# Performance work log

Measured on AMD Instinct MI355X. Metric: run time of the kernel, lower is better.

## Reference

```python
import jax, jax.numpy as jnp
import numpy as np

LAYER_SIZES = [256, 256, 256]
SPLIT_HALF = True
B, F0, D = 512, 32, 32


def setup_inputs() -> dict:
    key = jax.random.key(0)
    ks = jax.random.split(key, 7)
    field_nums = [F0]
    for i, s in enumerate(LAYER_SIZES):
        field_nums.append(s // 2 if (SPLIT_HALF and i != len(LAYER_SIZES) - 1) else (s // 2 if SPLIT_HALF else s))
    # field_nums = [32, 128, 128, 128] (last entry unused for weights)
    inp = {
        'feat': jax.random.normal(ks[0], (B, F0, D), dtype=jnp.float32),
        'W0': jax.random.normal(ks[1], (LAYER_SIZES[0], field_nums[0], F0), dtype=jnp.float32) * 0.05,
        'b0': jnp.zeros((LAYER_SIZES[0],), dtype=jnp.float32),
        'W1': jax.random.normal(ks[2], (LAYER_SIZES[1], field_nums[1], F0), dtype=jnp.float32) * 0.05,
        'b1': jnp.zeros((LAYER_SIZES[1],), dtype=jnp.float32),
        'W2': jax.random.normal(ks[3], (LAYER_SIZES[2], field_nums[2], F0), dtype=jnp.float32) * 0.05,
        'b2': jnp.zeros((LAYER_SIZES[2],), dtype=jnp.float32),
    }
    return inp


def _cin_layer(h, feat, W, b):
    # h: [B,H,D], feat: [B,F0,D], W: [K,H,F0], b: [K] -> out [B,K,D]
    # outer product per embedding dim, then 1x1 conv (full [H,F0] contraction)
    z = jnp.einsum('bid,bjd->bdij', h, feat)          # [B,D,H,F0]
    out = jnp.einsum('bdij,kij->bkd', z, W) + b[None, :, None]
    return jax.nn.relu(out)


def reference(feat, W0, b0, W1, b1, W2, b2):
    Ws = [W0, W1, W2]
    bs = [b0, b1, b2]
    h = feat
    p = []
    n_layers = len(LAYER_SIZES)
    for l, K in enumerate(LAYER_SIZES):
        out = _cin_layer(h, feat, Ws[l], bs[l])        # [B,K,D]
        if SPLIT_HALF and l != n_layers - 1:
            h = out[:, :K // 2, :]
            direct = out[:, K // 2:, :]
        else:
            direct = out
            h = out
        p.append(direct)
    return jnp.concatenate(p, axis=1).sum(-1)          # [B, sum of direct sizes]
```

## Files before the change

kernel.cpp:

```cpp
#include <hip/hip_runtime.h>
#include <hip/hip_fp16.h>
#include <stdint.h>


typedef _Float16 half8_t __attribute__((ext_vector_type(8)));
typedef float f32x4 __attribute__((ext_vector_type(4)));
typedef uint32_t u32x4 __attribute__((ext_vector_type(4)));

union H8 {
  half8_t h;
  uint32_t u[4];
  u32x4 q;
};

#define AS1 __attribute__((address_space(1)))
#define AS3 __attribute__((address_space(3)))

static __device__ __forceinline__ uint32_t pkmul(uint32_t x, uint32_t y) {
  __half2 a = __builtin_bit_cast(__half2, x);
  __half2 b = __builtin_bit_cast(__half2, y);
  __half2 r = __hmul2(a, b);
  return __builtin_bit_cast(uint32_t, r);
}

__global__ void prep_kernel(const float* __restrict__ W0, const float* __restrict__ W1,
                            const float* __restrict__ W2, const float* __restrict__ feat,
                            uint16_t* __restrict__ Wt0, uint16_t* __restrict__ Wt1,
                            uint16_t* __restrict__ Wt2,
                            uint16_t* __restrict__ F16, uint16_t* __restrict__ Fpk) {
  int blk = blockIdx.x;
  if (blk < 4608) {
    const float* W; uint16_t* Wt; int FLsh, base;
    if (blk < 512)       { W = W0; Wt = Wt0; FLsh = 5; base = 0; }
    else if (blk < 2560) { W = W1; Wt = Wt1; FLsh = 7; base = 512; }
    else                 { W = W2; Wt = Wt2; FLsh = 7; base = 2560; }
    int idx2 = (blk - base) * 256 + threadIdx.x;
    float2 xy = *(const float2*)(W + (size_t)idx2 * 2);
    int j2 = idx2 & 15;
    int i = (idx2 >> 4) & ((1 << FLsh) - 1);
    int k = idx2 >> (4 + FLsh);
    __half2 h2 = __floats2half2_rn(xy.x, xy.y);
    int g = j2 >> 2, kr = k & 15, kt = k >> 4;
    uint32_t* wt32 = (uint32_t*)Wt;
    wt32[(((size_t)i * 16 + kt) * 64 + g * 16 + kr) * 4 + (j2 & 3)] = *(uint32_t*)&h2;
  } else {
    int m = (blk - 4608) * 256 + threadIdx.x;
    int b = m >> 5, d = m & 31;
    const float* fb = feat + (size_t)b * 1024 + d;
    uint16_t hs[32];
#pragma unroll
    for (int j = 0; j < 32; ++j)
      hs[j] = __half_as_ushort(__float2half(fb[j * 32]));
    int mt = m >> 6, g = (m >> 5) & 1, plr = m & 15, hf = (m >> 4) & 1;
#pragma unroll
    for (int j = 0; j < 32; ++j)
      Fpk[(((size_t)mt * 32 + j) * 32 + plr * 2 + g) * 2 + hf] = hs[j];
#pragma unroll
    for (int c = 0; c < 4; ++c) {
      u32x4 q;
      q[0] = (uint32_t)hs[c * 8 + 0] | ((uint32_t)hs[c * 8 + 1] << 16);
      q[1] = (uint32_t)hs[c * 8 + 2] | ((uint32_t)hs[c * 8 + 3] << 16);
      q[2] = (uint32_t)hs[c * 8 + 4] | ((uint32_t)hs[c * 8 + 5] << 16);
      q[3] = (uint32_t)hs[c * 8 + 6] | ((uint32_t)hs[c * 8 + 7] << 16);
      *(u32x4*)(F16 + (size_t)m * 32 + c * 8) = q;
    }
  }
}

__global__ __launch_bounds__(1024) void gemm_cin(
    const uint32_t* __restrict__ hsrc,
    int hblock,
    const uint16_t* __restrict__ wt,
    const uint16_t* __restrict__ f16m,
    const float* __restrict__ bias,
    uint32_t* __restrict__ hout,
    float* __restrict__ outp,
    int FL, int obase, int klo) {
  __shared__ __align__(16) char smem[131072];
  const int tid = threadIdx.x;
  const int lane = tid & 63, w = tid >> 6;
  const int lr = lane & 15, hi = lane >> 4;
  const int bx = blockIdx.x;
  const int mg = bx >> 4, kg = bx & 15;
  const int mt = mg * 16 + w;
  const int m0 = mt * 64;
  const int FLm = FL - 1;

  const char* wbase = (const char*)wt + kg * 1024;
  for (int qq = tid; qq < FL * 64; qq += 1024) {
    __builtin_amdgcn_global_load_lds(
        (const AS1 uint32_t*)(wbase + (size_t)(qq >> 6) * 16384 + (qq & 63) * 16),
        (AS3 uint32_t*)(smem + (size_t)qq * 16), 16, 0, 0);
  }

  H8 ff[4];
#pragma unroll
  for (int mf = 0; mf < 4; ++mf)
    ff[mf].q = *(const u32x4*)(f16m + (size_t)(m0 + mf * 16 + lr) * 32 + hi * 8);

  const uint32_t* hb = hsrc + (size_t)mt * hblock + lr * 2;
  uint2 hq0 = *(const uint2*)(hb + 0 * 32);
  uint2 hq1 = *(const uint2*)(hb + (1 & FLm) * 32);
  uint2 hq2 = *(const uint2*)(hb + (2 & FLm) * 32);
  uint2 hq3 = *(const uint2*)(hb + (3 & FLm) * 32);

  f32x4 acc[4];
#pragma unroll
  for (int mf = 0; mf < 4; ++mf) acc[mf] = (f32x4){0.f, 0.f, 0.f, 0.f};

  asm volatile("s_waitcnt vmcnt(0)" ::: "memory");
  __syncthreads();

#define CIN_STEP(IDX, HQ)                                                      \
  {                                                                            \
    const int i_ = (IDX);                                                      \
    H8 wf;                                                                     \
    wf.q = *(const u32x4*)(smem + (size_t)i_ * 1024 + lane * 16);              \
    uint32_t e0 = __builtin_amdgcn_perm(HQ.x, HQ.x, 0x01000100u);              \
    uint32_t e1 = __builtin_amdgcn_perm(HQ.x, HQ.x, 0x03020302u);              \
    uint32_t e2 = __builtin_amdgcn_perm(HQ.y, HQ.y, 0x01000100u);              \
    uint32_t e3 = __builtin_amdgcn_perm(HQ.y, HQ.y, 0x03020302u);              \
    HQ = *(const uint2*)(hb + ((i_ + 4) & FLm) * 32);                          \
    H8 a0, a1, a2, a3;                                                         \
    _Pragma("unroll")                                                          \
    for (int c = 0; c < 4; ++c) {                                              \
      a0.u[c] = pkmul(ff[0].u[c], e0);                                         \
      a1.u[c] = pkmul(ff[1].u[c], e1);                                         \
      a2.u[c] = pkmul(ff[2].u[c], e2);                                         \
      a3.u[c] = pkmul(ff[3].u[c], e3);                                         \
    }                                                                          \
    acc[0] = __builtin_amdgcn_mfma_f32_16x16x32_f16(wf.h, a0.h, acc[0], 0, 0, 0); \
    acc[1] = __builtin_amdgcn_mfma_f32_16x16x32_f16(wf.h, a1.h, acc[1], 0, 0, 0); \
    acc[2] = __builtin_amdgcn_mfma_f32_16x16x32_f16(wf.h, a2.h, acc[2], 0, 0, 0); \
    acc[3] = __builtin_amdgcn_mfma_f32_16x16x32_f16(wf.h, a3.h, acc[3], 0, 0, 0); \
  }

  for (int t = 0; t < FL; t += 4) {
    CIN_STEP(t + 0, hq0)
    CIN_STEP(t + 1, hq1)
    CIN_STEP(t + 2, hq2)
    CIN_STEP(t + 3, hq3)
  }
#undef CIN_STEP

  f32x4 bv = *(const f32x4*)(bias + kg * 16 + hi * 4);
  float v[4][4];
#pragma unroll
  for (int mf = 0; mf < 4; ++mf)
#pragma unroll
    for (int r = 0; r < 4; ++r) {
      float x = acc[mf][r] + bv[r];
      v[mf][r] = x > 0.f ? x : 0.f;
    }

  if (hout != nullptr && kg < 8) {
#pragma unroll
    for (int r = 0; r < 4; ++r) {
      int k = kg * 16 + hi * 4 + r;
#pragma unroll
      for (int g = 0; g < 2; ++g) {
        uint32_t lo = __half_as_ushort(__float2half(v[2 * g][r]));
        uint32_t hi16 = __half_as_ushort(__float2half(v[2 * g + 1][r]));
        hout[(size_t)mt * 4096 + k * 32 + lr * 2 + g] = lo | (hi16 << 16);
      }
    }
  }

  f32x4 s0v, s1v;
#pragma unroll
  for (int r = 0; r < 4; ++r) {
    float x0 = v[0][r] + v[1][r];
    x0 += __shfl_xor(x0, 1); x0 += __shfl_xor(x0, 2);
    x0 += __shfl_xor(x0, 4); x0 += __shfl_xor(x0, 8);
    s0v[r] = x0;
    float x1 = v[2][r] + v[3][r];
    x1 += __shfl_xor(x1, 1); x1 += __shfl_xor(x1, 2);
    x1 += __shfl_xor(x1, 4); x1 += __shfl_xor(x1, 8);
    s1v[r] = x1;
  }
  int k0 = kg * 16 + hi * 4;
  if (lr == 0 && k0 >= klo) {
    *(f32x4*)(outp + (size_t)(mt * 2) * 512 + obase + k0 - klo) = s0v;
    *(f32x4*)(outp + (size_t)(mt * 2 + 1) * 512 + obase + k0 - klo) = s1v;
  }
}

extern "C" void kernel_launch(void* const* d_in, const int* in_sizes, int n_in,
                              void* d_out, int out_size, void* d_ws, size_t ws_size,
                              hipStream_t stream) {
  const float* feat = (const float*)d_in[0];
  const float* W0 = (const float*)d_in[1];
  const float* b0 = (const float*)d_in[2];
  const float* W1 = (const float*)d_in[3];
  const float* b1 = (const float*)d_in[4];
  const float* W2 = (const float*)d_in[5];
  const float* b2 = (const float*)d_in[6];
  float* out = (float*)d_out;
  char* ws = (char*)d_ws;

  uint16_t* Wt0 = (uint16_t*)(ws + 0x000000);
  uint16_t* Wt1 = (uint16_t*)(ws + 0x080000);
  uint16_t* Wt2 = (uint16_t*)(ws + 0x280000);
  uint16_t* F16 = (uint16_t*)(ws + 0x480000);
  uint16_t* Fpk = (uint16_t*)(ws + 0x580000);
  uint32_t* h1  = (uint32_t*)(ws + 0x680000);
  uint32_t* h2  = (uint32_t*)(ws + 0xA80000);

  prep_kernel<<<4672, 256, 0, stream>>>(W0, W1, W2, feat, Wt0, Wt1, Wt2, F16, Fpk);

  gemm_cin<<<256, 1024, 0, stream>>>((const uint32_t*)Fpk, 1024, Wt0, F16, b0,
                                     h1, out, 32, 0, 128);
  gemm_cin<<<256, 1024, 0, stream>>>(h1, 4096, Wt1, F16, b1,
                                     h2, out, 128, 128, 128);
  gemm_cin<<<256, 1024, 0, stream>>>(h2, 4096, Wt2, F16, b2,
                                     (uint32_t*)nullptr, out, 128, 256, 0);
}
```

Measured before the change: 100.8 us.

## Store h pre-duplicated per lane and software-pipeline LDS weight loads

```diff
diff --git a/kernel.cpp b/kernel.cpp
--- a/kernel.cpp
+++ b/kernel.cpp
@@ -27,7 +27,7 @@
                             const float* __restrict__ W2, const float* __restrict__ feat,
                             uint16_t* __restrict__ Wt0, uint16_t* __restrict__ Wt1,
                             uint16_t* __restrict__ Wt2,
-                            uint16_t* __restrict__ F16, uint16_t* __restrict__ Fpk) {
+                            uint16_t* __restrict__ F16, uint32_t* __restrict__ Fdup) {
   int blk = blockIdx.x;
   if (blk < 4608) {
     const float* W; uint16_t* Wt; int FLsh, base;
@@ -51,10 +51,14 @@
 #pragma unroll
     for (int j = 0; j < 32; ++j)
       hs[j] = __half_as_ushort(__float2half(fb[j * 32]));
-    int mt = m >> 6, g = (m >> 5) & 1, plr = m & 15, hf = (m >> 4) & 1;
-#pragma unroll
-    for (int j = 0; j < 32; ++j)
-      Fpk[(((size_t)mt * 32 + j) * 32 + plr * 2 + g) * 2 + hf] = hs[j];
+    int mt = m >> 6, mf = (m >> 4) & 3, l2 = m & 15;
+    uint32_t* Fd = Fdup + (size_t)mt * 2304 + l2 * 4 + mf;
+#pragma unroll
+    for (int j = 0; j < 32; ++j) {
+      uint32_t du = (uint32_t)hs[j] * 0x10001u;
+      Fd[j * 64] = du;
+      if (j < 4) Fd[(32 + j) * 64] = du;
+    }
 #pragma unroll
     for (int c = 0; c < 4; ++c) {
       u32x4 q;
@@ -67,16 +71,16 @@
   }
 }
 
-__global__ __launch_bounds__(1024) void gemm_cin(
-    const uint32_t* __restrict__ hsrc,
-    int hblock,
+__global__ __launch_bounds__(1024, 4) void gemm_cin(
+    const uint32_t* __restrict__ hdup,
+    int hstride,
     const uint16_t* __restrict__ wt,
     const uint16_t* __restrict__ f16m,
     const float* __restrict__ bias,
     uint32_t* __restrict__ hout,
     float* __restrict__ outp,
     int FL, int obase, int klo) {
-  __shared__ __align__(16) char smem[131072];
+  __shared__ __align__(16) char smem[134144];
   const int tid = threadIdx.x;
   const int lane = tid & 63, w = tid >> 6;
   const int lr = lane & 15, hi = lane >> 4;
@@ -87,9 +91,11 @@
   const int FLm = FL - 1;
 
   const char* wbase = (const char*)wt + kg * 1024;
-  for (int qq = tid; qq < FL * 64; qq += 1024) {
+  const int nq = (FL + 3) * 64;
+  for (int qq = tid; qq < nq; qq += 1024) {
+    int sl = (qq >> 6) & FLm;
     __builtin_amdgcn_global_load_lds(
-        (const AS1 uint32_t*)(wbase + (size_t)(qq >> 6) * 16384 + (qq & 63) * 16),
+        (const AS1 uint32_t*)(wbase + (size_t)sl * 16384 + (qq & 63) * 16),
         (AS3 uint32_t*)(smem + (size_t)qq * 16), 16, 0, 0);
   }
 
@@ -98,11 +104,11 @@
   for (int mf = 0; mf < 4; ++mf)
     ff[mf].q = *(const u32x4*)(f16m + (size_t)(m0 + mf * 16 + lr) * 32 + hi * 8);
 
-  const uint32_t* hb = hsrc + (size_t)mt * hblock + lr * 2;
-  uint2 hq0 = *(const uint2*)(hb + 0 * 32);
-  uint2 hq1 = *(const uint2*)(hb + (1 & FLm) * 32);
-  uint2 hq2 = *(const uint2*)(hb + (2 & FLm) * 32);
-  uint2 hq3 = *(const uint2*)(hb + (3 & FLm) * 32);
+  const uint32_t* hb = hdup + (size_t)mt * hstride + lr * 4;
+  u32x4 hrA = *(const u32x4*)(hb + 0 * 64);
+  u32x4 hrB = *(const u32x4*)(hb + 1 * 64);
+  u32x4 hrC = *(const u32x4*)(hb + 2 * 64);
+  u32x4 hrD = *(const u32x4*)(hb + 3 * 64);
 
   f32x4 acc[4];
 #pragma unroll
@@ -111,35 +117,36 @@
   asm volatile("s_waitcnt vmcnt(0)" ::: "memory");
   __syncthreads();
 
-#define CIN_STEP(IDX, HQ)                                                      \
-  {                                                                            \
-    const int i_ = (IDX);                                                      \
-    H8 wf;                                                                     \
-    wf.q = *(const u32x4*)(smem + (size_t)i_ * 1024 + lane * 16);              \
-    uint32_t e0 = __builtin_amdgcn_perm(HQ.x, HQ.x, 0x01000100u);              \
-    uint32_t e1 = __builtin_amdgcn_perm(HQ.x, HQ.x, 0x03020302u);              \
-    uint32_t e2 = __builtin_amdgcn_perm(HQ.y, HQ.y, 0x01000100u);              \
-    uint32_t e3 = __builtin_amdgcn_perm(HQ.y, HQ.y, 0x03020302u);              \
-    HQ = *(const uint2*)(hb + ((i_ + 4) & FLm) * 32);                          \
-    H8 a0, a1, a2, a3;                                                         \
-    _Pragma("unroll")                                                          \
-    for (int c = 0; c < 4; ++c) {                                              \
-      a0.u[c] = pkmul(ff[0].u[c], e0);                                         \
-      a1.u[c] = pkmul(ff[1].u[c], e1);                                         \
-      a2.u[c] = pkmul(ff[2].u[c], e2);                                         \
-      a3.u[c] = pkmul(ff[3].u[c], e3);                                         \
-    }                                                                          \
-    acc[0] = __builtin_amdgcn_mfma_f32_16x16x32_f16(wf.h, a0.h, acc[0], 0, 0, 0); \
-    acc[1] = __builtin_amdgcn_mfma_f32_16x16x32_f16(wf.h, a1.h, acc[1], 0, 0, 0); \
-    acc[2] = __builtin_amdgcn_mfma_f32_16x16x32_f16(wf.h, a2.h, acc[2], 0, 0, 0); \
-    acc[3] = __builtin_amdgcn_mfma_f32_16x16x32_f16(wf.h, a3.h, acc[3], 0, 0, 0); \
+  H8 wr0, wr1, wr2, wr3;
+  wr0.q = *(const u32x4*)(smem + 0 * 1024 + lane * 16);
+  wr1.q = *(const u32x4*)(smem + 1 * 1024 + lane * 16);
+  wr2.q = *(const u32x4*)(smem + 2 * 1024 + lane * 16);
+
+#define CIN_STEP(WRC, HRC, WRN, WOFF, HOFF)                                        \
+  {                                                                                \
+    uint32_t e0 = HRC[0], e1 = HRC[1], e2 = HRC[2], e3 = HRC[3];                   \
+    WRN.q = *(const u32x4*)(wls + (WOFF) * 1024);                                  \
+    HRC = *(const u32x4*)(hpt + (HOFF) * 64);                                      \
+    H8 a0, a1, a2, a3;                                                             \
+    _Pragma("unroll") for (int c = 0; c < 4; ++c) {                                \
+      a0.u[c] = pkmul(ff[0].u[c], e0);                                             \
+      a1.u[c] = pkmul(ff[1].u[c], e1);                                             \
+      a2.u[c] = pkmul(ff[2].u[c], e2);                                             \
+      a3.u[c] = pkmul(ff[3].u[c], e3);                                             \
+    }                                                                              \
+    acc[0] = __builtin_amdgcn_mfma_f32_16x16x32_f16(WRC.h, a0.h, acc[0], 0, 0, 0); \
+    acc[1] = __builtin_amdgcn_mfma_f32_16x16x32_f16(WRC.h, a1.h, acc[1], 0, 0, 0); \
+    acc[2] = __builtin_amdgcn_mfma_f32_16x16x32_f16(WRC.h, a2.h, acc[2], 0, 0, 0); \
+    acc[3] = __builtin_amdgcn_mfma_f32_16x16x32_f16(WRC.h, a3.h, acc[3], 0, 0, 0); \
   }
 
   for (int t = 0; t < FL; t += 4) {
-    CIN_STEP(t + 0, hq0)
-    CIN_STEP(t + 1, hq1)
-    CIN_STEP(t + 2, hq2)
-    CIN_STEP(t + 3, hq3)
+    const char* wls = smem + (size_t)t * 1024 + lane * 16;
+    const uint32_t* hpt = hb + (size_t)t * 64;
+    CIN_STEP(wr0, hrA, wr3, 3, 4)
+    CIN_STEP(wr1, hrB, wr0, 4, 5)
+    CIN_STEP(wr2, hrC, wr1, 5, 6)
+    CIN_STEP(wr3, hrD, wr2, 6, 7)
   }
 #undef CIN_STEP
 
@@ -157,12 +164,13 @@
 #pragma unroll
     for (int r = 0; r < 4; ++r) {
       int k = kg * 16 + hi * 4 + r;
-#pragma unroll
-      for (int g = 0; g < 2; ++g) {
-        uint32_t lo = __half_as_ushort(__float2half(v[2 * g][r]));
-        uint32_t hi16 = __half_as_ushort(__float2half(v[2 * g + 1][r]));
-        hout[(size_t)mt * 4096 + k * 32 + lr * 2 + g] = lo | (hi16 << 16);
-      }
+      uint32_t* hp = hout + ((size_t)mt * 132 + k) * 64 + lr * 4;
+      u32x4 du;
+#pragma unroll
+      for (int mf = 0; mf < 4; ++mf)
+        du[mf] = (uint32_t)__half_as_ushort(__float2half(v[mf][r])) * 0x10001u;
+      *(u32x4*)hp = du;
+      if (kg == 0 && hi == 0) *(u32x4*)(hp + 8192) = du;
     }
   }
 
@@ -198,20 +206,18 @@
   float* out = (float*)d_out;
   char* ws = (char*)d_ws;
 
-  uint16_t* Wt0 = (uint16_t*)(ws + 0x000000);
-  uint16_t* Wt1 = (uint16_t*)(ws + 0x080000);
-  uint16_t* Wt2 = (uint16_t*)(ws + 0x280000);
-  uint16_t* F16 = (uint16_t*)(ws + 0x480000);
-  uint16_t* Fpk = (uint16_t*)(ws + 0x580000);
-  uint32_t* h1  = (uint32_t*)(ws + 0x680000);
-  uint32_t* h2  = (uint32_t*)(ws + 0xA80000);
-
-  prep_kernel<<<4672, 256, 0, stream>>>(W0, W1, W2, feat, Wt0, Wt1, Wt2, F16, Fpk);
-
-  gemm_cin<<<256, 1024, 0, stream>>>((const uint32_t*)Fpk, 1024, Wt0, F16, b0,
-                                     h1, out, 32, 0, 128);
-  gemm_cin<<<256, 1024, 0, stream>>>(h1, 4096, Wt1, F16, b1,
-                                     h2, out, 128, 128, 128);
-  gemm_cin<<<256, 1024, 0, stream>>>(h2, 4096, Wt2, F16, b2,
-                                     (uint32_t*)nullptr, out, 128, 256, 0);
-}
+  uint16_t* Wt0  = (uint16_t*)(ws + 0x000000);
+  uint16_t* Wt1  = (uint16_t*)(ws + 0x080000);
+  uint16_t* Wt2  = (uint16_t*)(ws + 0x280000);
+  uint16_t* F16  = (uint16_t*)(ws + 0x480000);
+  uint32_t* Fdup = (uint32_t*)(ws + 0x580000);
+  uint32_t* h1   = (uint32_t*)(ws + 0x800000);
+  uint32_t* h2   = (uint32_t*)(ws + 0x1100000);
+
+  prep_kernel<<<4672, 256, 0, stream>>>(W0, W1, W2, feat, Wt0, Wt1, Wt2, F16, Fdup);
+
+  gemm_cin<<<256, 1024, 0, stream>>>(Fdup, 2304, Wt0, F16, b0, h1, out, 32, 0, 128);
+  gemm_cin<<<256, 1024, 0, stream>>>(h1, 8448, Wt1, F16, b1, h2, out, 128, 128, 128);
+  gemm_cin<<<256, 1024, 0, stream>>>(h2, 8448, Wt2, F16, b2, (uint32_t*)nullptr,
+                                     out, 128, 256, 0);
+}
```

Measured after the change: 100.5 us. No clear change (-0.3%).

## Switch CIN GEMM to 32x32 MFMA tiles with double-buffered weight staging

Applied to the files above, without the earlier changes.

```diff
diff --git a/kernel.cpp b/kernel.cpp
--- a/kernel.cpp
+++ b/kernel.cpp
@@ -5,6 +5,7 @@
 
 typedef _Float16 half8_t __attribute__((ext_vector_type(8)));
 typedef float f32x4 __attribute__((ext_vector_type(4)));
+typedef float f32x16 __attribute__((ext_vector_type(16)));
 typedef uint32_t u32x4 __attribute__((ext_vector_type(4)));
 
 union H8 {
@@ -23,11 +24,16 @@
   return __builtin_bit_cast(uint32_t, r);
 }
 
+static __device__ __forceinline__ uint32_t pack2h(float a, float b) {
+  __half2 r = __floats2half2_rn(a, b);
+  return __builtin_bit_cast(uint32_t, r);
+}
+
 __global__ void prep_kernel(const float* __restrict__ W0, const float* __restrict__ W1,
                             const float* __restrict__ W2, const float* __restrict__ feat,
                             uint16_t* __restrict__ Wt0, uint16_t* __restrict__ Wt1,
                             uint16_t* __restrict__ Wt2,
-                            uint16_t* __restrict__ F16, uint16_t* __restrict__ Fpk) {
+                            uint16_t* __restrict__ F16, uint32_t* __restrict__ hP0) {
   int blk = blockIdx.x;
   if (blk < 4608) {
     const float* W; uint16_t* Wt; int FLsh, base;
@@ -51,10 +57,12 @@
 #pragma unroll
     for (int j = 0; j < 32; ++j)
       hs[j] = __half_as_ushort(__float2half(fb[j * 32]));
-    int mt = m >> 6, g = (m >> 5) & 1, plr = m & 15, hf = (m >> 4) & 1;
-#pragma unroll
-    for (int j = 0; j < 32; ++j)
-      Fpk[(((size_t)mt * 32 + j) * 32 + plr * 2 + g) * 2 + hf] = hs[j];
+    int mb = m >> 5, ml = m & 31;
+#pragma unroll
+    for (int jp = 0; jp < 16; ++jp) {
+      uint32_t pr = (uint32_t)hs[2 * jp] | ((uint32_t)hs[2 * jp + 1] << 16);
+      hP0[((size_t)(mb * 4 + (jp >> 2)) * 32 + ml) * 4 + (jp & 3)] = pr;
+    }
 #pragma unroll
     for (int c = 0; c < 4; ++c) {
       u32x4 q;
@@ -67,121 +75,135 @@
   }
 }
 
-__global__ __launch_bounds__(1024) void gemm_cin(
-    const uint32_t* __restrict__ hsrc,
-    int hblock,
+template <int FL>
+__global__ __launch_bounds__(1024, 4) void gemm_cin(
+    const uint32_t* __restrict__ hP,
     const uint16_t* __restrict__ wt,
     const uint16_t* __restrict__ f16m,
     const float* __restrict__ bias,
-    uint32_t* __restrict__ hout,
+    uint32_t* __restrict__ houtP,
     float* __restrict__ outp,
-    int FL, int obase, int klo) {
+    int obase, int klo) {
   __shared__ __align__(16) char smem[131072];
   const int tid = threadIdx.x;
   const int lane = tid & 63, w = tid >> 6;
-  const int lr = lane & 15, hi = lane >> 4;
+  const int l31 = lane & 31, l5 = lane >> 5;
   const int bx = blockIdx.x;
-  const int mg = bx >> 4, kg = bx & 15;
-  const int mt = mg * 16 + w;
-  const int m0 = mt * 64;
-  const int FLm = FL - 1;
-
-  const char* wbase = (const char*)wt + kg * 1024;
-  for (int qq = tid; qq < FL * 64; qq += 1024) {
-    __builtin_amdgcn_global_load_lds(
-        (const AS1 uint32_t*)(wbase + (size_t)(qq >> 6) * 16384 + (qq & 63) * 16),
-        (AS3 uint32_t*)(smem + (size_t)qq * 16), 16, 0, 0);
-  }
-
-  H8 ff[4];
-#pragma unroll
-  for (int mf = 0; mf < 4; ++mf)
-    ff[mf].q = *(const u32x4*)(f16m + (size_t)(m0 + mf * 16 + lr) * 32 + hi * 8);
-
-  const uint32_t* hb = hsrc + (size_t)mt * hblock + lr * 2;
-  uint2 hq0 = *(const uint2*)(hb + 0 * 32);
-  uint2 hq1 = *(const uint2*)(hb + (1 & FLm) * 32);
-  uint2 hq2 = *(const uint2*)(hb + (2 & FLm) * 32);
-  uint2 hq3 = *(const uint2*)(hb + (3 & FLm) * 32);
-
-  f32x4 acc[4];
-#pragma unroll
-  for (int mf = 0; mf < 4; ++mf) acc[mf] = (f32x4){0.f, 0.f, 0.f, 0.f};
-
-  asm volatile("s_waitcnt vmcnt(0)" ::: "memory");
+  const int kg = bx & 7, mg = bx >> 3;
+  const int mb = mg * 16 + w;
+
+  const uint16_t* fbase = f16m + (size_t)(mb * 32 + l31) * 32 + l5 * 8;
+  H8 ff0, ff1;
+  ff0.q = *(const u32x4*)(fbase);
+  ff1.q = *(const u32x4*)(fbase + 16);
+
+  const uint32_t* hbase = hP + (size_t)mb * (FL / 8) * 128 + l31 * 4;
+  u32x4 hqA[4], hqB[4];
+
+  const char* wsrc = (const char*)wt + kg * 2048;
+
+#define CIN_STAGE(QN, BUFOFS)                                                     \
+  _Pragma("unroll") for (int c_ = 0; c_ < 4; ++c_) {                              \
+    int u_ = w * 4 + c_;                                                          \
+    __builtin_amdgcn_global_load_lds(                                             \
+        (const AS1 uint32_t*)(wsrc + (size_t)((QN) * 32 + (u_ >> 1)) * 16384 +    \
+                              (u_ & 1) * 1024 + lane * 16),                       \
+        (AS3 uint32_t*)(smem + (BUFOFS) + u_ * 1024 + lane * 16), 16, 0, 0);      \
+  }
+
+#define CIN_HLOAD(QN, HQ)                                                         \
+  _Pragma("unroll") for (int c_ = 0; c_ < 4; ++c_)                                \
+      HQ[c_] = *(const u32x4*)(hbase + ((QN) * 4 + c_) * 128);
+
+  CIN_STAGE(0, 0)
+  CIN_HLOAD(0, hqA)
+
+  f32x16 acc = {};
+
+  const char* rb = smem + ((l31 >> 4) << 10) + (l5 << 8) + ((lane & 15) << 4);
+
   __syncthreads();
 
-#define CIN_STEP(IDX, HQ)                                                      \
-  {                                                                            \
-    const int i_ = (IDX);                                                      \
-    H8 wf;                                                                     \
-    wf.q = *(const u32x4*)(smem + (size_t)i_ * 1024 + lane * 16);              \
-    uint32_t e0 = __builtin_amdgcn_perm(HQ.x, HQ.x, 0x01000100u);              \
-    uint32_t e1 = __builtin_amdgcn_perm(HQ.x, HQ.x, 0x03020302u);              \
-    uint32_t e2 = __builtin_amdgcn_perm(HQ.y, HQ.y, 0x01000100u);              \
-    uint32_t e3 = __builtin_amdgcn_perm(HQ.y, HQ.y, 0x03020302u);              \
-    HQ = *(const uint2*)(hb + ((i_ + 4) & FLm) * 32);                          \
-    H8 a0, a1, a2, a3;                                                         \
-    _Pragma("unroll")                                                          \
-    for (int c = 0; c < 4; ++c) {                                              \
-      a0.u[c] = pkmul(ff[0].u[c], e0);                                         \
-      a1.u[c] = pkmul(ff[1].u[c], e1);                                         \
-      a2.u[c] = pkmul(ff[2].u[c], e2);                                         \
-      a3.u[c] = pkmul(ff[3].u[c], e3);                                         \
-    }                                                                          \
-    acc[0] = __builtin_amdgcn_mfma_f32_16x16x32_f16(wf.h, a0.h, acc[0], 0, 0, 0); \
-    acc[1] = __builtin_amdgcn_mfma_f32_16x16x32_f16(wf.h, a1.h, acc[1], 0, 0, 0); \
-    acc[2] = __builtin_amdgcn_mfma_f32_16x16x32_f16(wf.h, a2.h, acc[2], 0, 0, 0); \
-    acc[3] = __builtin_amdgcn_mfma_f32_16x16x32_f16(wf.h, a3.h, acc[3], 0, 0, 0); \
-  }
-
-  for (int t = 0; t < FL; t += 4) {
-    CIN_STEP(t + 0, hq0)
-    CIN_STEP(t + 1, hq1)
-    CIN_STEP(t + 2, hq2)
-    CIN_STEP(t + 3, hq3)
-  }
-#undef CIN_STEP
-
-  f32x4 bv = *(const f32x4*)(bias + kg * 16 + hi * 4);
-  float v[4][4];
-#pragma unroll
-  for (int mf = 0; mf < 4; ++mf)
-#pragma unroll
-    for (int r = 0; r < 4; ++r) {
-      float x = acc[mf][r] + bv[r];
-      v[mf][r] = x > 0.f ? x : 0.f;
+#define CIN_Q(HQ, RBOFS)                                                          \
+  {                                                                               \
+    const char* rb_ = rb + (RBOFS);                                               \
+    _Pragma("unroll") for (int s = 0; s < 32; ++s) {                              \
+      uint32_t hp_ = HQ[s >> 3][(s >> 1) & 3];                                    \
+      uint32_t e_ =                                                               \
+          __builtin_amdgcn_perm(hp_, hp_, (s & 1) ? 0x03020302u : 0x01000100u);   \
+      H8 wf0_, wf1_, b0_, b1_;                                                    \
+      wf0_.q = *(const u32x4*)(rb_ + s * 2048);                                   \
+      wf1_.q = *(const u32x4*)(rb_ + s * 2048 + 512);                             \
+      _Pragma("unroll") for (int c_ = 0; c_ < 4; ++c_) {                          \
+        b0_.u[c_] = pkmul(ff0.u[c_], e_);                                         \
+        b1_.u[c_] = pkmul(ff1.u[c_], e_);                                         \
+      }                                                                           \
+      __builtin_amdgcn_s_setprio(1);                                              \
+      acc = __builtin_amdgcn_mfma_f32_32x32x16_f16(wf0_.h, b0_.h, acc, 0, 0, 0);  \
+      acc = __builtin_amdgcn_mfma_f32_32x32x16_f16(wf1_.h, b1_.h, acc, 0, 0, 0);  \
+      __builtin_amdgcn_s_setprio(0);                                              \
+    }                                                                             \
+  }
+
+  if (FL == 32) {
+    CIN_Q(hqA, 0)
+  } else {
+    CIN_STAGE(1, 65536)
+    CIN_HLOAD(1, hqB)
+    CIN_Q(hqA, 0)
+    __syncthreads();
+    CIN_STAGE(2, 0)
+    CIN_HLOAD(2, hqA)
+    CIN_Q(hqB, 65536)
+    __syncthreads();
+    CIN_STAGE(3, 65536)
+    CIN_HLOAD(3, hqB)
+    CIN_Q(hqA, 0)
+    __syncthreads();
+    CIN_Q(hqB, 65536)
+  }
+#undef CIN_Q
+#undef CIN_STAGE
+#undef CIN_HLOAD
+
+  f32x4 bv[4];
+#pragma unroll
+  for (int a = 0; a < 4; ++a)
+    bv[a] = *(const f32x4*)(bias + kg * 32 + a * 8 + l5 * 4);
+  float v[16];
+#pragma unroll
+  for (int a = 0; a < 4; ++a)
+#pragma unroll
+    for (int t = 0; t < 4; ++t) {
+      float x = acc[a * 4 + t] + bv[a][t];
+      v[a * 4 + t] = x > 0.f ? x : 0.f;
     }
 
-  if (hout != nullptr && kg < 8) {
-#pragma unroll
-    for (int r = 0; r < 4; ++r) {
-      int k = kg * 16 + hi * 4 + r;
-#pragma unroll
-      for (int g = 0; g < 2; ++g) {
-        uint32_t lo = __half_as_ushort(__float2half(v[2 * g][r]));
-        uint32_t hi16 = __half_as_ushort(__float2half(v[2 * g + 1][r]));
-        hout[(size_t)mt * 4096 + k * 32 + lr * 2 + g] = lo | (hi16 << 16);
+  if (houtP != nullptr && kg < 4) {
+#pragma unroll
+    for (int a = 0; a < 4; ++a)
+#pragma unroll
+      for (int c = 0; c < 2; ++c) {
+        uint32_t pr = pack2h(v[a * 4 + 2 * c], v[a * 4 + 2 * c + 1]);
+        houtP[((size_t)(mb * 16 + kg * 4 + a) * 32 + l31) * 4 + 2 * l5 + c] = pr;
       }
-    }
-  }
-
-  f32x4 s0v, s1v;
-#pragma unroll
-  for (int r = 0; r < 4; ++r) {
-    float x0 = v[0][r] + v[1][r];
-    x0 += __shfl_xor(x0, 1); x0 += __shfl_xor(x0, 2);
-    x0 += __shfl_xor(x0, 4); x0 += __shfl_xor(x0, 8);
-    s0v[r] = x0;
-    float x1 = v[2][r] + v[3][r];
-    x1 += __shfl_xor(x1, 1); x1 += __shfl_xor(x1, 2);
-    x1 += __shfl_xor(x1, 4); x1 += __shfl_xor(x1, 8);
-    s1v[r] = x1;
-  }
-  int k0 = kg * 16 + hi * 4;
-  if (lr == 0 && k0 >= klo) {
-    *(f32x4*)(outp + (size_t)(mt * 2) * 512 + obase + k0 - klo) = s0v;
-    *(f32x4*)(outp + (size_t)(mt * 2 + 1) * 512 + obase + k0 - klo) = s1v;
+  }
+
+#pragma unroll
+  for (int r = 0; r < 16; ++r) {
+    float x = v[r];
+    x += __shfl_xor(x, 1);
+    x += __shfl_xor(x, 2);
+    x += __shfl_xor(x, 4);
+    x += __shfl_xor(x, 8);
+    x += __shfl_xor(x, 16);
+    v[r] = x;
+  }
+  if (kg * 32 >= klo && (lane == 0 || lane == 32)) {
+    float* ob = outp + (size_t)mb * 512 + obase + kg * 32 - klo + l5 * 4;
+#pragma unroll
+    for (int a = 0; a < 4; ++a)
+      *(f32x4*)(ob + a * 8) = (f32x4){v[a * 4], v[a * 4 + 1], v[a * 4 + 2], v[a * 4 + 3]};
   }
 }
 
@@ -202,16 +224,14 @@
   uint16_t* Wt1 = (uint16_t*)(ws + 0x080000);
   uint16_t* Wt2 = (uint16_t*)(ws + 0x280000);
   uint16_t* F16 = (uint16_t*)(ws + 0x480000);
-  uint16_t* Fpk = (uint16_t*)(ws + 0x580000);
-  uint32_t* h1  = (uint32_t*)(ws + 0x680000);
-  uint32_t* h2  = (uint32_t*)(ws + 0xA80000);
-
-  prep_kernel<<<4672, 256, 0, stream>>>(W0, W1, W2, feat, Wt0, Wt1, Wt2, F16, Fpk);
-
-  gemm_cin<<<256, 1024, 0, stream>>>((const uint32_t*)Fpk, 1024, Wt0, F16, b0,
-                                     h1, out, 32, 0, 128);
-  gemm_cin<<<256, 1024, 0, stream>>>(h1, 4096, Wt1, F16, b1,
-                                     h2, out, 128, 128, 128);
-  gemm_cin<<<256, 1024, 0, stream>>>(h2, 4096, Wt2, F16, b2,
-                                     (uint32_t*)nullptr, out, 128, 256, 0);
-}
+  uint32_t* hP0 = (uint32_t*)(ws + 0x580000);
+  uint32_t* hP1 = (uint32_t*)(ws + 0x680000);
+  uint32_t* hP2 = (uint32_t*)(ws + 0xA80000);
+
+  prep_kernel<<<4672, 256, 0, stream>>>(W0, W1, W2, feat, Wt0, Wt1, Wt2, F16, hP0);
+
+  gemm_cin<32><<<256, 1024, 0, stream>>>(hP0, Wt0, F16, b0, hP1, out, 0, 128);
+  gemm_cin<128><<<256, 1024, 0, stream>>>(hP1, Wt1, F16, b1, hP2, out, 128, 128);
+  gemm_cin<128><<<256, 1024, 0, stream>>>(hP2, Wt2, F16, b2, (uint32_t*)nullptr,
+                                          out, 256, 0);
+}
```

Measured after the change: 106.2 us. 5.3% more time.
